# Kernel optimization log

Measured on AMD Instinct MI355X. Metric: run time of the kernel, lower is better.

## Reference

```python
import jax, jax.numpy as jnp
import numpy as np

TEMP = 0.2
L_MAIN, L_VIEW, L_SUP, L_UNSUP = 1.0, 1.0, 1.0, 0.2
N, D, V, P, NEG, U = 100000, 256, 3, 1024, 1024, 2048


def setup_inputs() -> dict:
    key = jax.random.key(0)
    ks = jax.random.split(key, 8)
    fused_logit = jax.random.normal(ks[0], (N,), dtype=jnp.float32)
    view_logits = jax.random.normal(ks[1], (V, N), dtype=jnp.float32)
    proj = jax.random.normal(ks[2], (V, N, D), dtype=jnp.float32)
    proj = proj / jnp.linalg.norm(proj, axis=-1, keepdims=True)  # 'already normalized'
    labels = jax.random.randint(ks[3], (N,), 0, 2).astype(jnp.float32)
    train_mask = jax.random.randint(ks[4], (N,), 0, 2).astype(bool)
    train_pos_idx = jax.random.randint(ks[5], (P,), 0, N)
    train_neg_idx = jax.random.randint(ks[6], (NEG,), 0, N)
    unlabeled_idx = jax.random.randint(ks[7], (U,), 0, N)  # len == max_unsup_samples -> no subsampling
    return dict(fused_logit=fused_logit, view_logits=view_logits, proj=proj,
                labels=labels, train_mask=train_mask, train_pos_idx=train_pos_idx,
                train_neg_idx=train_neg_idx, unlabeled_idx=unlabeled_idx)


def _masked_bce(logits, labels, mask):
    # BCEWithLogitsLoss mean over masked elements (stable formulation)
    bce = jnp.maximum(logits, 0) - logits * labels + jnp.log1p(jnp.exp(-jnp.abs(logits)))
    mf = mask.astype(logits.dtype)
    return jnp.sum(bce * mf) / jnp.maximum(jnp.sum(mf), 1.0)


def _sup_contrastive(proj, pos_idx, neg_idx, temp):
    lab_idx = jnp.concatenate([pos_idx, neg_idx])
    node_labels = jnp.concatenate([jnp.ones(pos_idx.shape[0]), jnp.zeros(neg_idx.shape[0])])
    L = lab_idx.shape[0]
    Vv = proj.shape[0]
    z = proj[:, lab_idx, :].transpose(1, 0, 2)          # [L, V, D]
    zf = z.reshape(L * Vv, -1)                           # [L*V, D]
    sim = (zf @ zf.T) / temp                             # [L*V, L*V]
    sim = sim - jax.lax.stop_gradient(sim.max(axis=1, keepdims=True))
    es = jnp.exp(sim)
    node = jnp.repeat(jnp.arange(L), Vv)
    view = jnp.tile(jnp.arange(Vv), L)
    flab = jnp.repeat(node_labels, Vv)
    sn = node[:, None] == node[None, :]
    sv = view[:, None] == view[None, :]
    sl = flab[:, None] == flab[None, :]
    eye = jnp.eye(L * Vv, dtype=bool)
    pos_m = ((sn & ~sv) | (~sn & sl)) & ~eye
    neg_m = (~sn) & (~sl) & ~eye
    den_m = pos_m | neg_m
    denom = jnp.sum(es * den_m.astype(es.dtype), axis=1) + 1e-12
    posf = pos_m.astype(es.dtype)
    log_prob = -jnp.log((es * posf + 1e-12) / denom[:, None])
    pos_count = pos_m.sum(axis=1)
    loss_per_anchor = jnp.sum(log_prob * posf, axis=1) / (pos_count.astype(es.dtype) + 1e-12)
    valid = ((pos_count > 0) & (den_m.sum(axis=1) > 0)).astype(es.dtype)
    return jnp.sum(loss_per_anchor * valid) / jnp.maximum(jnp.sum(valid), 1.0)


def _unsup_consistency(proj, unl_idx, temp):
    # Vectorized form of the double python loop: full cosine-sim matrix with
    # masked denominator (all but self) and positives = same node, other views.
    Vv = proj.shape[0]
    z = proj[:, unl_idx, :].transpose(1, 0, 2)           # [U, V, D]
    Uu = z.shape[0]
    M = Uu * Vv
    zf = z.reshape(M, -1)
    zn = zf / (jnp.linalg.norm(zf, axis=1, keepdims=True) + 1e-8)
    es = jnp.exp((zn @ zn.T) / temp)                     # [M, M]
    denom = es.sum(axis=1) - jnp.diag(es) + 1e-12        # exclude self
    node = jnp.repeat(jnp.arange(Uu), Vv)
    view = jnp.tile(jnp.arange(Vv), Uu)
    pos_m = (node[:, None] == node[None, :]) & (view[:, None] != view[None, :])
    posf = pos_m.astype(es.dtype)
    log_prob = -jnp.log(es / denom[:, None])
    per_anchor = jnp.sum(log_prob * posf, axis=1) / (Vv - 1)
    return jnp.mean(per_anchor)


def reference(fused_logit, view_logits, proj, labels, train_mask,
              train_pos_idx, train_neg_idx, unlabeled_idx):
    main_loss = _masked_bce(fused_logit, labels, train_mask)
    view_loss = jnp.mean(jax.vmap(lambda lg: _masked_bce(lg, labels, train_mask))(view_logits))
    sup_loss = _sup_contrastive(proj, train_pos_idx, train_neg_idx, TEMP)
    unsup_loss = _unsup_consistency(proj, unlabeled_idx, TEMP)
    total = L_MAIN * main_loss + L_VIEW * view_loss + L_SUP * sup_loss + L_UNSUP * unsup_loss
    return jnp.stack([total, main_loss, view_loss, sup_loss, unsup_loss])
```

## Files before the change

kernel.cpp:

```cpp
#include <hip/hip_runtime.h>
#include <math.h>

typedef short short8 __attribute__((ext_vector_type(8)));
typedef float floatx4 __attribute__((ext_vector_type(4)));

#define TEMP_INV 5.0f
#define W_UNSUP 0.2f
#define NB_BCE 256
#define NSPLIT 8

static __device__ __forceinline__ unsigned short f2bf(float f) {
  unsigned int u = __float_as_uint(f);
  u += 0x7FFFu + ((u >> 16) & 1u);
  return (unsigned short)(u >> 16);
}

__device__ __forceinline__ float block_sum256(float v) {
  __shared__ float sh[4];
  for (int m = 1; m <= 32; m <<= 1) v += __shfl_xor(v, m);
  __syncthreads();
  if ((threadIdx.x & 63) == 0) sh[threadIdx.x >> 6] = v;
  __syncthreads();
  return sh[0] + sh[1] + sh[2] + sh[3];
}

__global__ __launch_bounds__(256) void bce_kernel(
    const float* __restrict__ fused, const float* __restrict__ viewl,
    const float* __restrict__ labels, const void* __restrict__ maskp,
    float* __restrict__ partials, int N, int V, int nw) {
  __shared__ int s_int, s_flt;
  const int t = threadIdx.x;
  if (t == 0) { s_int = 1; s_flt = 1; }
  __syncthreads();
  {
    const unsigned int* w = (const unsigned int*)maskp;
    int okI = 1, okF = 1;
    for (int i = t; i < nw; i += 256) {
      unsigned int x = w[i];
      if (x != 0u && x != 1u) okI = 0;
      if (x != 0u && x != 0x3F800000u) okF = 0;
    }
    if (!okI) atomicAnd(&s_int, 0);
    if (!okF) atomicAnd(&s_flt, 0);
  }
  __syncthreads();
  const int flag = s_int ? 0 : (s_flt ? 1 : 2);

  float cnt = 0.f, sm = 0.f;
  float sv[8];
  for (int v = 0; v < 8; v++) sv[v] = 0.f;
  const int Vc = V > 8 ? 8 : V;
  for (int i = blockIdx.x * blockDim.x + t; i < N; i += gridDim.x * blockDim.x) {
    bool m;
    if (flag == 0)      m = ((const int*)maskp)[i] != 0;
    else if (flag == 1) m = ((const float*)maskp)[i] != 0.0f;
    else                m = ((const unsigned char*)maskp)[i] != 0;
    if (!m) continue;
    float y = labels[i];
    cnt += 1.0f;
    float x = fused[i];
    sm += fmaxf(x, 0.f) - x * y + log1pf(__expf(-fabsf(x)));
    for (int v = 0; v < Vc; v++) {
      float xv = viewl[(size_t)v * N + i];
      sv[v] += fmaxf(xv, 0.f) - xv * y + log1pf(__expf(-fabsf(xv)));
    }
  }
  float tot = block_sum256(cnt);
  if (t == 0) partials[blockIdx.x * 16 + 0] = tot;
  tot = block_sum256(sm);
  if (t == 0) partials[blockIdx.x * 16 + 1] = tot;
  for (int v = 0; v < Vc; v++) {
    tot = block_sum256(sv[v]);
    if (t == 0) partials[blockIdx.x * 16 + 2 + v] = tot;
  }
}

__global__ __launch_bounds__(256) void gather_kernel(
    const float* __restrict__ proj, const int* __restrict__ pos_idx,
    const int* __restrict__ neg_idx, const int* __restrict__ unl_idx,
    unsigned short* __restrict__ zsup, unsigned short* __restrict__ zuns,
    float* __restrict__ dsup, float* __restrict__ duns,
    float* __restrict__ Esup, float* __restrict__ Bsup,
    float* __restrict__ Euns, float* __restrict__ Buns,
    int N, int D, int V, int P, int Msup, int Muns) {
  const int prob = blockIdx.y;
  const int M = prob ? Muns : Msup;
  const int r0 = blockIdx.x * 8;
  const int t = threadIdx.x;
  if (t < 8) {
    int rz = r0 + t;
    if (rz < M) {
      if (prob) { Euns[rz] = 0.f; Buns[rz] = 0.f; }
      else      { Esup[rz] = 0.f; Bsup[rz] = 0.f; }
    }
  }
  const int sub = t >> 5, ln = t & 31;
  const int r = r0 + sub;
  if (r >= M) return;
  const int l = r / V, v = r - l * V;
  const int idx = prob ? unl_idx[l] : (l < P ? pos_idx[l] : neg_idx[l - P]);
  const float* src = proj + ((size_t)v * N + (size_t)idx) * D + ln * 8;
  floatx4 p0 = *(const floatx4*)(src);
  floatx4 p1 = *(const floatx4*)(src + 4);
  float s = 0.f;
#pragma unroll
  for (int k = 0; k < 4; k++) s += p0[k] * p0[k] + p1[k] * p1[k];
  for (int m = 1; m <= 16; m <<= 1) s += __shfl_xor(s, m);
  const float n2 = s;
  float sc = 1.0f, dval = n2 * TEMP_INV;
  if (prob) {
    sc = 1.0f / (sqrtf(n2) + 1e-8f);
    dval = n2 * sc * sc * TEMP_INV;
  }
  short8 vv;
#pragma unroll
  for (int k = 0; k < 4; k++) {
    vv[k]     = (short)f2bf(p0[k] * sc);
    vv[k + 4] = (short)f2bf(p1[k] * sc);
  }
  unsigned short* zd = prob ? zuns : zsup;
  *(short8*)(zd + (size_t)r * 256 + ln * 8) = vv;
  if (ln == 0) (prob ? duns : dsup)[r] = dval;
}

__global__ __launch_bounds__(256) void sim_kernel(
    const unsigned short* __restrict__ zsup, const unsigned short* __restrict__ zuns,
    float* __restrict__ Esup, float* __restrict__ Bsup,
    float* __restrict__ Euns, float* __restrict__ Buns,
    int Msup, int Muns, int PV, int V, int nsSup, int nsUns) {
  const int prob = blockIdx.y;
  const unsigned short* __restrict__ z = prob ? zuns : zsup;
  float* __restrict__ Ep = prob ? Euns : Esup;
  float* __restrict__ Bp = prob ? Buns : Bsup;
  const int M = prob ? Muns : Msup;
  const int ns = prob ? nsUns : nsSup;

  const int si = blockIdx.x / NSPLIT;
  const int s  = blockIdx.x - si * NSPLIT;
  if (si >= ns) return;

  const int R0 = si * 64;
  const int tid = threadIdx.x;
  const int wave = tid >> 6;
  const int wr = wave >> 1, wc = wave & 1;
  const int q = (tid >> 4) & 3;
  const int n16 = tid & 15;

  __shared__ __align__(16) unsigned short lds[64 * 264];

  const int srow = tid >> 5;
  const int soff = (tid & 31) * 8;

  short8 a[2][8];
#pragma unroll
  for (int m = 0; m < 2; m++) {
    int row = R0 + wr * 32 + m * 16 + n16;
    if (row >= M) row = M - 1;
    const unsigned short* zr = z + (size_t)row * 256 + q * 8;
#pragma unroll
    for (int ks = 0; ks < 8; ks++) a[m][ks] = *(const short8*)(zr + ks * 32);
  }

  int bs[2][4], be[2][4];
#pragma unroll
  for (int m = 0; m < 2; m++)
#pragma unroll
    for (int r = 0; r < 4; r++) {
      int row = R0 + wr * 32 + m * 16 + q * 4 + r;
      if (row >= M) row = M - 1;
      if (prob == 0) { bs[m][r] = row < PV ? 0 : PV; be[m][r] = row < PV ? PV : M; }
      else           { int b0 = (row / V) * V; bs[m][r] = b0; be[m][r] = b0 + V; }
    }

  float er0[4] = {0, 0, 0, 0}, er1[4] = {0, 0, 0, 0};
  float br0[4] = {0, 0, 0, 0}, br1[4] = {0, 0, 0, 0};

  short8 cur[8];
  int tj = si + s;
  if (tj < ns) {
    const int C0 = tj * 64;
#pragma unroll
    for (int cc = 0; cc < 8; cc++) {
      int gcol = C0 + srow + cc * 8;
      short8 vv = {0, 0, 0, 0, 0, 0, 0, 0};
      if (gcol < M) vv = *(const short8*)(z + (size_t)gcol * 256 + soff);
      cur[cc] = vv;
    }
  }

  for (; tj < ns; tj += NSPLIT) {
    const int C0 = tj * 64;
    __syncthreads();
#pragma unroll
    for (int cc = 0; cc < 8; cc++)
      *(short8*)(&lds[(srow + cc * 8) * 264 + soff]) = cur[cc];
    {
      int tjn = tj + NSPLIT;
      if (tjn < ns) {
        const int C0n = tjn * 64;
#pragma unroll
        for (int cc = 0; cc < 8; cc++) {
          int gcol = C0n + srow + cc * 8;
          short8 vv = {0, 0, 0, 0, 0, 0, 0, 0};
          if (gcol < M) vv = *(const short8*)(z + (size_t)gcol * 256 + soff);
          cur[cc] = vv;
        }
      }
    }
    __syncthreads();

    floatx4 acc00 = {0.f, 0.f, 0.f, 0.f}, acc01 = {0.f, 0.f, 0.f, 0.f};
    floatx4 acc10 = {0.f, 0.f, 0.f, 0.f}, acc11 = {0.f, 0.f, 0.f, 0.f};
#pragma unroll
    for (int ks = 0; ks < 8; ks++) {
      const unsigned short* bp = &lds[(wc * 32 + n16) * 264 + q * 8 + ks * 32];
      short8 b0 = *(const short8*)bp;
      short8 b1 = *(const short8*)(bp + 16 * 264);
      acc00 = __builtin_amdgcn_mfma_f32_16x16x32_bf16(a[0][ks], b0, acc00, 0, 0, 0);
      acc01 = __builtin_amdgcn_mfma_f32_16x16x32_bf16(a[0][ks], b1, acc01, 0, 0, 0);
      acc10 = __builtin_amdgcn_mfma_f32_16x16x32_bf16(a[1][ks], b0, acc10, 0, 0, 0);
      acc11 = __builtin_amdgcn_mfma_f32_16x16x32_bf16(a[1][ks], b1, acc11, 0, 0, 0);
    }

    float ec0 = 0.f, ec1 = 0.f, bc0 = 0.f, bc1 = 0.f;
    const int j0 = C0 + wc * 32 + n16;
    const int j1 = j0 + 16;

#define EPI(ACC, MM, JN, ECOL, BCOL, ERA, BRA)                        \
  _Pragma("unroll")                                                   \
  for (int r = 0; r < 4; r++) {                                       \
    int row = R0 + wr * 32 + MM * 16 + q * 4 + r;                     \
    float tv = ACC[r] * TEMP_INV;                                     \
    bool valid = (row < M) && (JN < M);                               \
    float e = valid ? __expf(tv - 5.0f) : 0.0f;                       \
    float bv = (valid && JN >= bs[MM][r] && JN < be[MM][r]) ? tv : 0.0f; \
    ERA[r] += e; BRA[r] += bv; ECOL += e; BCOL += bv;                 \
  }
    EPI(acc00, 0, j0, ec0, bc0, er0, br0)
    EPI(acc01, 0, j1, ec1, bc1, er0, br0)
    EPI(acc10, 1, j0, ec0, bc0, er1, br1)
    EPI(acc11, 1, j1, ec1, bc1, er1, br1)
#undef EPI

    if (tj != si) {
      float e = ec0, b = bc0;
      e += __shfl_xor(e, 16); e += __shfl_xor(e, 32);
      b += __shfl_xor(b, 16); b += __shfl_xor(b, 32);
      if (q == 0 && j0 < M) { atomicAdd(&Ep[j0], e); atomicAdd(&Bp[j0], b); }
      e = ec1; b = bc1;
      e += __shfl_xor(e, 16); e += __shfl_xor(e, 32);
      b += __shfl_xor(b, 16); b += __shfl_xor(b, 32);
      if (q == 0 && j1 < M) { atomicAdd(&Ep[j1], e); atomicAdd(&Bp[j1], b); }
    }
  }

#pragma unroll
  for (int mr = 0; mr < 8; mr++) {
    const int m = mr >> 2, r = mr & 3;
    float e = m ? er1[r] : er0[r];
    float b = m ? br1[r] : br0[r];
    for (int msk = 1; msk <= 8; msk <<= 1) { e += __shfl_xor(e, msk); b += __shfl_xor(b, msk); }
    int row = R0 + wr * 32 + m * 16 + q * 4 + r;
    if (n16 == 0 && row < M) {
      atomicAdd(&Ep[row], e);
      atomicAdd(&Bp[row], b);
    }
  }
}

__global__ __launch_bounds__(256) void finalize_kernel(
    const float* __restrict__ partials,
    const float* __restrict__ Esup, const float* __restrict__ Bsup, const float* __restrict__ dsup,
    const float* __restrict__ Euns, const float* __restrict__ Buns, const float* __restrict__ duns,
    int Msup, int Muns, int PV, int P, int NEG, int V, float* __restrict__ out) {
  const int t = threadIdx.x;
  float cnt = 0.f, sm = 0.f, sv[8];
  for (int v = 0; v < 8; v++) sv[v] = 0.f;
  const int Vc = V > 8 ? 8 : V;
  for (int b = t; b < NB_BCE; b += 256) {
    cnt += partials[b * 16 + 0];
    sm  += partials[b * 16 + 1];
    for (int v = 0; v < Vc; v++) sv[v] += partials[b * 16 + 2 + v];
  }
  cnt = block_sum256(cnt);
  sm = block_sum256(sm);
  float svt = 0.f;
  for (int v = 0; v < Vc; v++) svt += block_sum256(sv[v]);
  const float denomC = fmaxf(cnt, 1.0f);
  const float main_loss = sm / denomC;
  const float view_loss = (svt / denomC) / (float)V;

  float ssup = 0.f;
  for (int row = t; row < Msup; row += 256) {
    float E = Esup[row], B = Bsup[row];
    float d = dsup[row];
    float dn = E - __expf(d - 5.0f);
    float cl = (row < PV) ? (float)P : (float)NEG;
    float pc = (float)(V - 1) + (cl - 1.0f) * (float)V;
    ssup += logf(dn) + 5.0f - (B - d) / pc;
  }
  ssup = block_sum256(ssup);
  const float sup_loss = ssup / (float)Msup;

  float suns = 0.f;
  for (int row = t; row < Muns; row += 256) {
    float E = Euns[row], B = Buns[row];
    float d = duns[row];
    float dn = E - __expf(d - 5.0f);
    suns += logf(dn) + 5.0f - (B - d) / (float)(V - 1);
  }
  suns = block_sum256(suns);
  const float unsup_loss = suns / (float)Muns;

  if (t == 0) {
    float total = main_loss + view_loss + sup_loss + W_UNSUP * unsup_loss;
    out[0] = total;
    out[1] = main_loss;
    out[2] = view_loss;
    out[3] = sup_loss;
    out[4] = unsup_loss;
  }
}

extern "C" void kernel_launch(void* const* d_in, const int* in_sizes, int n_in,
                              void* d_out, int out_size, void* d_ws, size_t ws_size,
                              hipStream_t stream) {
  const float* fused  = (const float*)d_in[0];
  const float* viewl  = (const float*)d_in[1];
  const float* proj   = (const float*)d_in[2];
  const float* labels = (const float*)d_in[3];
  const void*  maskp  = d_in[4];
  const int* pos_idx  = (const int*)d_in[5];
  const int* neg_idx  = (const int*)d_in[6];
  const int* unl_idx  = (const int*)d_in[7];

  const int N = in_sizes[0];
  const int V = in_sizes[1] / N;
  const int D = in_sizes[2] / in_sizes[1];
  const int P = in_sizes[5];
  const int NEG = in_sizes[6];
  const int U = in_sizes[7];
  const int L = P + NEG;
  const int Msup = L * V;
  const int Muns = U * V;
  const int PV = P * V;

  char* ws = (char*)d_ws;
  size_t off = 0;
  auto alloc = [&](size_t bytes) { size_t o = off; off += (bytes + 255) & ~(size_t)255; return o; };
  const size_t o_part = alloc((size_t)NB_BCE * 16 * 4);
  const size_t o_zsup = alloc((size_t)Msup * D * 2);
  const size_t o_zuns = alloc((size_t)Muns * D * 2);
  const size_t o_dsup = alloc((size_t)Msup * 4);
  const size_t o_duns = alloc((size_t)Muns * 4);
  const size_t o_Esup = alloc((size_t)Msup * 4);
  const size_t o_Bsup = alloc((size_t)Msup * 4);
  const size_t o_Euns = alloc((size_t)Muns * 4);
  const size_t o_Buns = alloc((size_t)Muns * 4);

  float* partials = (float*)(ws + o_part);
  unsigned short* zsup = (unsigned short*)(ws + o_zsup);
  unsigned short* zuns = (unsigned short*)(ws + o_zuns);
  float* dsup = (float*)(ws + o_dsup);
  float* duns = (float*)(ws + o_duns);
  float* Esup = (float*)(ws + o_Esup);
  float* Bsup = (float*)(ws + o_Bsup);
  float* Euns = (float*)(ws + o_Euns);
  float* Buns = (float*)(ws + o_Buns);

  int nw = N / 4 < 256 ? N / 4 : 256;
  bce_kernel<<<NB_BCE, 256, 0, stream>>>(fused, viewl, labels, maskp, partials, N, V, nw);

  const int Mmax = Msup > Muns ? Msup : Muns;
  dim3 ggrid((Mmax + 7) / 8, 2);
  gather_kernel<<<ggrid, 256, 0, stream>>>(proj, pos_idx, neg_idx, unl_idx,
                                           zsup, zuns, dsup, duns,
                                           Esup, Bsup, Euns, Buns,
                                           N, D, V, P, Msup, Muns);

  const int nsS = (Msup + 63) / 64;
  const int nsU = (Muns + 63) / 64;
  const int nsMax = nsS > nsU ? nsS : nsU;
  dim3 sgrid(nsMax * NSPLIT, 2);
  sim_kernel<<<sgrid, 256, 0, stream>>>(zsup, zuns, Esup, Bsup, Euns, Buns,
                                        Msup, Muns, PV, V, nsS, nsU);

  finalize_kernel<<<1, 256, 0, stream>>>(partials, Esup, Bsup, dsup, Euns, Buns, duns,
                                         Msup, Muns, PV, P, NEG, V, (float*)d_out);
}
```

Before: 445.3 us.

## Merge BCE and gather kernels; fold finalize into sim via last-block ticket

The BCE reduction and the gather/normalize step become a single prep kernel, with blocks partitioned by index. The finalize reduction moves into the tail of the similarity kernel: each block takes an atomic ticket, and the last block to finish computes the final losses using coherent loads. Four launches become two, removing launch overhead and inter-kernel gaps. In exchange every sim block pays for an extra atomic and fence, and the final reduction runs on a single block at the end of the kernel.

```diff
diff --git a/kernel.cpp b/kernel.cpp
--- a/kernel.cpp
+++ b/kernel.cpp
@@ -13,6 +13,10 @@
   unsigned int u = __float_as_uint(f);
   u += 0x7FFFu + ((u >> 16) & 1u);
   return (unsigned short)(u >> 16);
+}
+
+static __device__ __forceinline__ float coh_load(const float* p) {
+  return __hip_atomic_load(p, __ATOMIC_RELAXED, __HIP_MEMORY_SCOPE_AGENT);
 }
 
 __device__ __forceinline__ float block_sum256(float v) {
@@ -24,69 +28,74 @@
   return sh[0] + sh[1] + sh[2] + sh[3];
 }
 
-__global__ __launch_bounds__(256) void bce_kernel(
+__global__ __launch_bounds__(256) void prep_kernel(
     const float* __restrict__ fused, const float* __restrict__ viewl,
     const float* __restrict__ labels, const void* __restrict__ maskp,
-    float* __restrict__ partials, int N, int V, int nw) {
-  __shared__ int s_int, s_flt;
-  const int t = threadIdx.x;
-  if (t == 0) { s_int = 1; s_flt = 1; }
-  __syncthreads();
-  {
-    const unsigned int* w = (const unsigned int*)maskp;
-    int okI = 1, okF = 1;
-    for (int i = t; i < nw; i += 256) {
-      unsigned int x = w[i];
-      if (x != 0u && x != 1u) okI = 0;
-      if (x != 0u && x != 0x3F800000u) okF = 0;
-    }
-    if (!okI) atomicAnd(&s_int, 0);
-    if (!okF) atomicAnd(&s_flt, 0);
-  }
-  __syncthreads();
-  const int flag = s_int ? 0 : (s_flt ? 1 : 2);
-
-  float cnt = 0.f, sm = 0.f;
-  float sv[8];
-  for (int v = 0; v < 8; v++) sv[v] = 0.f;
-  const int Vc = V > 8 ? 8 : V;
-  for (int i = blockIdx.x * blockDim.x + t; i < N; i += gridDim.x * blockDim.x) {
-    bool m;
-    if (flag == 0)      m = ((const int*)maskp)[i] != 0;
-    else if (flag == 1) m = ((const float*)maskp)[i] != 0.0f;
-    else                m = ((const unsigned char*)maskp)[i] != 0;
-    if (!m) continue;
-    float y = labels[i];
-    cnt += 1.0f;
-    float x = fused[i];
-    sm += fmaxf(x, 0.f) - x * y + log1pf(__expf(-fabsf(x)));
-    for (int v = 0; v < Vc; v++) {
-      float xv = viewl[(size_t)v * N + i];
-      sv[v] += fmaxf(xv, 0.f) - xv * y + log1pf(__expf(-fabsf(xv)));
-    }
-  }
-  float tot = block_sum256(cnt);
-  if (t == 0) partials[blockIdx.x * 16 + 0] = tot;
-  tot = block_sum256(sm);
-  if (t == 0) partials[blockIdx.x * 16 + 1] = tot;
-  for (int v = 0; v < Vc; v++) {
-    tot = block_sum256(sv[v]);
-    if (t == 0) partials[blockIdx.x * 16 + 2 + v] = tot;
-  }
-}
-
-__global__ __launch_bounds__(256) void gather_kernel(
+    float* __restrict__ partials, int N, int V, int nw,
     const float* __restrict__ proj, const int* __restrict__ pos_idx,
     const int* __restrict__ neg_idx, const int* __restrict__ unl_idx,
     unsigned short* __restrict__ zsup, unsigned short* __restrict__ zuns,
     float* __restrict__ dsup, float* __restrict__ duns,
     float* __restrict__ Esup, float* __restrict__ Bsup,
     float* __restrict__ Euns, float* __restrict__ Buns,
-    int N, int D, int V, int P, int Msup, int Muns) {
-  const int prob = blockIdx.y;
+    int D, int P, int Msup, int Muns, int gblocks,
+    unsigned int* __restrict__ ticket) {
+  const int bx = blockIdx.x;
+  const int t = threadIdx.x;
+  if (bx == 0 && t == 0) *ticket = 0u;
+
+  if (bx < NB_BCE) {
+    __shared__ int s_int, s_flt;
+    if (t == 0) { s_int = 1; s_flt = 1; }
+    __syncthreads();
+    {
+      const unsigned int* w = (const unsigned int*)maskp;
+      int okI = 1, okF = 1;
+      for (int i = t; i < nw; i += 256) {
+        unsigned int x = w[i];
+        if (x != 0u && x != 1u) okI = 0;
+        if (x != 0u && x != 0x3F800000u) okF = 0;
+      }
+      if (!okI) atomicAnd(&s_int, 0);
+      if (!okF) atomicAnd(&s_flt, 0);
+    }
+    __syncthreads();
+    const int flag = s_int ? 0 : (s_flt ? 1 : 2);
+
+    float cnt = 0.f, sm = 0.f;
+    float sv[8];
+    for (int v = 0; v < 8; v++) sv[v] = 0.f;
+    const int Vc = V > 8 ? 8 : V;
+    for (int i = bx * 256 + t; i < N; i += NB_BCE * 256) {
+      bool m;
+      if (flag == 0)      m = ((const int*)maskp)[i] != 0;
+      else if (flag == 1) m = ((const float*)maskp)[i] != 0.0f;
+      else                m = ((const unsigned char*)maskp)[i] != 0;
+      if (!m) continue;
+      float y = labels[i];
+      cnt += 1.0f;
+      float x = fused[i];
+      sm += fmaxf(x, 0.f) - x * y + log1pf(__expf(-fabsf(x)));
+      for (int v = 0; v < Vc; v++) {
+        float xv = viewl[(size_t)v * N + i];
+        sv[v] += fmaxf(xv, 0.f) - xv * y + log1pf(__expf(-fabsf(xv)));
+      }
+    }
+    float tot = block_sum256(cnt);
+    if (t == 0) partials[bx * 16 + 0] = tot;
+    tot = block_sum256(sm);
+    if (t == 0) partials[bx * 16 + 1] = tot;
+    for (int v = 0; v < Vc; v++) {
+      tot = block_sum256(sv[v]);
+      if (t == 0) partials[bx * 16 + 2 + v] = tot;
+    }
+    return;
+  }
+
+  const int g = bx - NB_BCE;
+  const int prob = g >= gblocks ? 1 : 0;
   const int M = prob ? Muns : Msup;
-  const int r0 = blockIdx.x * 8;
-  const int t = threadIdx.x;
+  const int r0 = (g - prob * gblocks) * 8;
   if (t < 8) {
     int rz = r0 + t;
     if (rz < M) {
@@ -127,7 +136,10 @@
     const unsigned short* __restrict__ zsup, const unsigned short* __restrict__ zuns,
     float* __restrict__ Esup, float* __restrict__ Bsup,
     float* __restrict__ Euns, float* __restrict__ Buns,
-    int Msup, int Muns, int PV, int V, int nsSup, int nsUns) {
+    int Msup, int Muns, int PV, int V, int nsSup, int nsUns,
+    const float* __restrict__ partials,
+    const float* __restrict__ dsup, const float* __restrict__ duns,
+    int P, int NEG, float* __restrict__ out, unsigned int* __restrict__ ticket) {
   const int prob = blockIdx.y;
   const unsigned short* __restrict__ z = prob ? zuns : zsup;
   float* __restrict__ Ep = prob ? Euns : Esup;
@@ -137,94 +149,95 @@
 
   const int si = blockIdx.x / NSPLIT;
   const int s  = blockIdx.x - si * NSPLIT;
-  if (si >= ns) return;
-
-  const int R0 = si * 64;
+
   const int tid = threadIdx.x;
-  const int wave = tid >> 6;
-  const int wr = wave >> 1, wc = wave & 1;
-  const int q = (tid >> 4) & 3;
-  const int n16 = tid & 15;
 
   __shared__ __align__(16) unsigned short lds[64 * 264];
 
-  const int srow = tid >> 5;
-  const int soff = (tid & 31) * 8;
-
-  short8 a[2][8];
-#pragma unroll
-  for (int m = 0; m < 2; m++) {
-    int row = R0 + wr * 32 + m * 16 + n16;
-    if (row >= M) row = M - 1;
-    const unsigned short* zr = z + (size_t)row * 256 + q * 8;
-#pragma unroll
-    for (int ks = 0; ks < 8; ks++) a[m][ks] = *(const short8*)(zr + ks * 32);
-  }
-
-  int bs[2][4], be[2][4];
-#pragma unroll
-  for (int m = 0; m < 2; m++)
-#pragma unroll
-    for (int r = 0; r < 4; r++) {
-      int row = R0 + wr * 32 + m * 16 + q * 4 + r;
+  if (si < ns) {
+    const int R0 = si * 64;
+    const int wave = tid >> 6;
+    const int wr = wave >> 1, wc = wave & 1;
+    const int q = (tid >> 4) & 3;
+    const int n16 = tid & 15;
+
+    const int srow = tid >> 5;
+    const int soff = (tid & 31) * 8;
+
+    short8 a[2][8];
+#pragma unroll
+    for (int m = 0; m < 2; m++) {
+      int row = R0 + wr * 32 + m * 16 + n16;
       if (row >= M) row = M - 1;
-      if (prob == 0) { bs[m][r] = row < PV ? 0 : PV; be[m][r] = row < PV ? PV : M; }
-      else           { int b0 = (row / V) * V; bs[m][r] = b0; be[m][r] = b0 + V; }
-    }
-
-  float er0[4] = {0, 0, 0, 0}, er1[4] = {0, 0, 0, 0};
-  float br0[4] = {0, 0, 0, 0}, br1[4] = {0, 0, 0, 0};
-
-  short8 cur[8];
-  int tj = si + s;
-  if (tj < ns) {
-    const int C0 = tj * 64;
-#pragma unroll
-    for (int cc = 0; cc < 8; cc++) {
-      int gcol = C0 + srow + cc * 8;
-      short8 vv = {0, 0, 0, 0, 0, 0, 0, 0};
-      if (gcol < M) vv = *(const short8*)(z + (size_t)gcol * 256 + soff);
-      cur[cc] = vv;
-    }
-  }
-
-  for (; tj < ns; tj += NSPLIT) {
-    const int C0 = tj * 64;
-    __syncthreads();
-#pragma unroll
-    for (int cc = 0; cc < 8; cc++)
-      *(short8*)(&lds[(srow + cc * 8) * 264 + soff]) = cur[cc];
-    {
-      int tjn = tj + NSPLIT;
-      if (tjn < ns) {
-        const int C0n = tjn * 64;
-#pragma unroll
-        for (int cc = 0; cc < 8; cc++) {
-          int gcol = C0n + srow + cc * 8;
-          short8 vv = {0, 0, 0, 0, 0, 0, 0, 0};
-          if (gcol < M) vv = *(const short8*)(z + (size_t)gcol * 256 + soff);
-          cur[cc] = vv;
+      const unsigned short* zr = z + (size_t)row * 256 + q * 8;
+#pragma unroll
+      for (int ks = 0; ks < 8; ks++) a[m][ks] = *(const short8*)(zr + ks * 32);
+    }
+
+    int bs[2][4], be[2][4];
+#pragma unroll
+    for (int m = 0; m < 2; m++)
+#pragma unroll
+      for (int r = 0; r < 4; r++) {
+        int row = R0 + wr * 32 + m * 16 + q * 4 + r;
+        if (row >= M) row = M - 1;
+        if (prob == 0) { bs[m][r] = row < PV ? 0 : PV; be[m][r] = row < PV ? PV : M; }
+        else           { int b0 = (row / V) * V; bs[m][r] = b0; be[m][r] = b0 + V; }
+      }
+
+    float er0[4] = {0, 0, 0, 0}, er1[4] = {0, 0, 0, 0};
+    float br0[4] = {0, 0, 0, 0}, br1[4] = {0, 0, 0, 0};
+
+    short8 cur[8];
+    int tj = si + s;
+    if (tj < ns) {
+      const int C0 = tj * 64;
+#pragma unroll
+      for (int cc = 0; cc < 8; cc++) {
+        int gcol = C0 + srow + cc * 8;
+        short8 vv = {0, 0, 0, 0, 0, 0, 0, 0};
+        if (gcol < M) vv = *(const short8*)(z + (size_t)gcol * 256 + soff);
+        cur[cc] = vv;
+      }
+    }
+
+    for (; tj < ns; tj += NSPLIT) {
+      const int C0 = tj * 64;
+      __syncthreads();
+#pragma unroll
+      for (int cc = 0; cc < 8; cc++)
+        *(short8*)(&lds[(srow + cc * 8) * 264 + soff]) = cur[cc];
+      {
+        int tjn = tj + NSPLIT;
+        if (tjn < ns) {
+          const int C0n = tjn * 64;
+#pragma unroll
+          for (int cc = 0; cc < 8; cc++) {
+            int gcol = C0n + srow + cc * 8;
+            short8 vv = {0, 0, 0, 0, 0, 0, 0, 0};
+            if (gcol < M) vv = *(const short8*)(z + (size_t)gcol * 256 + soff);
+            cur[cc] = vv;
+          }
         }
       }
-    }
-    __syncthreads();
-
-    floatx4 acc00 = {0.f, 0.f, 0.f, 0.f}, acc01 = {0.f, 0.f, 0.f, 0.f};
-    floatx4 acc10 = {0.f, 0.f, 0.f, 0.f}, acc11 = {0.f, 0.f, 0.f, 0.f};
-#pragma unroll
-    for (int ks = 0; ks < 8; ks++) {
-      const unsigned short* bp = &lds[(wc * 32 + n16) * 264 + q * 8 + ks * 32];
-      short8 b0 = *(const short8*)bp;
-      short8 b1 = *(const short8*)(bp + 16 * 264);
-      acc00 = __builtin_amdgcn_mfma_f32_16x16x32_bf16(a[0][ks], b0, acc00, 0, 0, 0);
-      acc01 = __builtin_amdgcn_mfma_f32_16x16x32_bf16(a[0][ks], b1, acc01, 0, 0, 0);
-      acc10 = __builtin_amdgcn_mfma_f32_16x16x32_bf16(a[1][ks], b0, acc10, 0, 0, 0);
-      acc11 = __builtin_amdgcn_mfma_f32_16x16x32_bf16(a[1][ks], b1, acc11, 0, 0, 0);
-    }
-
-    float ec0 = 0.f, ec1 = 0.f, bc0 = 0.f, bc1 = 0.f;
-    const int j0 = C0 + wc * 32 + n16;
-    const int j1 = j0 + 16;
+      __syncthreads();
+
+      floatx4 acc00 = {0.f, 0.f, 0.f, 0.f}, acc01 = {0.f, 0.f, 0.f, 0.f};
+      floatx4 acc10 = {0.f, 0.f, 0.f, 0.f}, acc11 = {0.f, 0.f, 0.f, 0.f};
+#pragma unroll
+      for (int ks = 0; ks < 8; ks++) {
+        const unsigned short* bp = &lds[(wc * 32 + n16) * 264 + q * 8 + ks * 32];
+        short8 b0 = *(const short8*)bp;
+        short8 b1 = *(const short8*)(bp + 16 * 264);
+        acc00 = __builtin_amdgcn_mfma_f32_16x16x32_bf16(a[0][ks], b0, acc00, 0, 0, 0);
+        acc01 = __builtin_amdgcn_mfma_f32_16x16x32_bf16(a[0][ks], b1, acc01, 0, 0, 0);
+        acc10 = __builtin_amdgcn_mfma_f32_16x16x32_bf16(a[1][ks], b0, acc10, 0, 0, 0);
+        acc11 = __builtin_amdgcn_mfma_f32_16x16x32_bf16(a[1][ks], b1, acc11, 0, 0, 0);
+      }
+
+      float ec0 = 0.f, ec1 = 0.f, bc0 = 0.f, bc1 = 0.f;
+      const int j0 = C0 + wc * 32 + n16;
+      const int j1 = j0 + 16;
 
 #define EPI(ACC, MM, JN, ECOL, BCOL, ERA, BRA)                        \
   _Pragma("unroll")                                                   \
@@ -236,44 +249,49 @@
     float bv = (valid && JN >= bs[MM][r] && JN < be[MM][r]) ? tv : 0.0f; \
     ERA[r] += e; BRA[r] += bv; ECOL += e; BCOL += bv;                 \
   }
-    EPI(acc00, 0, j0, ec0, bc0, er0, br0)
-    EPI(acc01, 0, j1, ec1, bc1, er0, br0)
-    EPI(acc10, 1, j0, ec0, bc0, er1, br1)
-    EPI(acc11, 1, j1, ec1, bc1, er1, br1)
+      EPI(acc00, 0, j0, ec0, bc0, er0, br0)
+      EPI(acc01, 0, j1, ec1, bc1, er0, br0)
+      EPI(acc10, 1, j0, ec0, bc0, er1, br1)
+      EPI(acc11, 1, j1, ec1, bc1, er1, br1)
 #undef EPI
 
-    if (tj != si) {
-      float e = ec0, b = bc0;
-      e += __shfl_xor(e, 16); e += __shfl_xor(e, 32);
-      b += __shfl_xor(b, 16); b += __shfl_xor(b, 32);
-      if (q == 0 && j0 < M) { atomicAdd(&Ep[j0], e); atomicAdd(&Bp[j0], b); }
-      e = ec1; b = bc1;
-      e += __shfl_xor(e, 16); e += __shfl_xor(e, 32);
-      b += __shfl_xor(b, 16); b += __shfl_xor(b, 32);
-      if (q == 0 && j1 < M) { atomicAdd(&Ep[j1], e); atomicAdd(&Bp[j1], b); }
-    }
-  }
-
-#pragma unroll
-  for (int mr = 0; mr < 8; mr++) {
-    const int m = mr >> 2, r = mr & 3;
-    float e = m ? er1[r] : er0[r];
-    float b = m ? br1[r] : br0[r];
-    for (int msk = 1; msk <= 8; msk <<= 1) { e += __shfl_xor(e, msk); b += __shfl_xor(b, msk); }
-    int row = R0 + wr * 32 + m * 16 + q * 4 + r;
-    if (n16 == 0 && row < M) {
-      atomicAdd(&Ep[row], e);
-      atomicAdd(&Bp[row], b);
-    }
-  }
-}
-
-__global__ __launch_bounds__(256) void finalize_kernel(
-    const float* __restrict__ partials,
-    const float* __restrict__ Esup, const float* __restrict__ Bsup, const float* __restrict__ dsup,
-    const float* __restrict__ Euns, const float* __restrict__ Buns, const float* __restrict__ duns,
-    int Msup, int Muns, int PV, int P, int NEG, int V, float* __restrict__ out) {
-  const int t = threadIdx.x;
+      if (tj != si) {
+        float e = ec0, b = bc0;
+        e += __shfl_xor(e, 16); e += __shfl_xor(e, 32);
+        b += __shfl_xor(b, 16); b += __shfl_xor(b, 32);
+        if (q == 0 && j0 < M) { atomicAdd(&Ep[j0], e); atomicAdd(&Bp[j0], b); }
+        e = ec1; b = bc1;
+        e += __shfl_xor(e, 16); e += __shfl_xor(e, 32);
+        b += __shfl_xor(b, 16); b += __shfl_xor(b, 32);
+        if (q == 0 && j1 < M) { atomicAdd(&Ep[j1], e); atomicAdd(&Bp[j1], b); }
+      }
+    }
+
+#pragma unroll
+    for (int mr = 0; mr < 8; mr++) {
+      const int m = mr >> 2, r = mr & 3;
+      float e = m ? er1[r] : er0[r];
+      float b = m ? br1[r] : br0[r];
+      for (int msk = 1; msk <= 8; msk <<= 1) { e += __shfl_xor(e, msk); b += __shfl_xor(b, msk); }
+      int row = R0 + wr * 32 + m * 16 + q * 4 + r;
+      if (n16 == 0 && row < M) {
+        atomicAdd(&Ep[row], e);
+        atomicAdd(&Bp[row], b);
+      }
+    }
+  }
+
+  __shared__ int isLast;
+  if (tid == 0) {
+    __threadfence();
+    unsigned int old = atomicAdd(ticket, 1u);
+    isLast = (old == gridDim.x * gridDim.y - 1u) ? 1 : 0;
+  }
+  __syncthreads();
+  if (!isLast) return;
+  __threadfence();
+
+  const int t = tid;
   float cnt = 0.f, sm = 0.f, sv[8];
   for (int v = 0; v < 8; v++) sv[v] = 0.f;
   const int Vc = V > 8 ? 8 : V;
@@ -292,7 +310,7 @@
 
   float ssup = 0.f;
   for (int row = t; row < Msup; row += 256) {
-    float E = Esup[row], B = Bsup[row];
+    float E = coh_load(&Esup[row]), B = coh_load(&Bsup[row]);
     float d = dsup[row];
     float dn = E - __expf(d - 5.0f);
     float cl = (row < PV) ? (float)P : (float)NEG;
@@ -304,7 +322,7 @@
 
   float suns = 0.f;
   for (int row = t; row < Muns; row += 256) {
-    float E = Euns[row], B = Buns[row];
+    float E = coh_load(&Euns[row]), B = coh_load(&Buns[row]);
     float d = duns[row];
     float dn = E - __expf(d - 5.0f);
     suns += logf(dn) + 5.0f - (B - d) / (float)(V - 1);
@@ -357,6 +375,7 @@
   const size_t o_Bsup = alloc((size_t)Msup * 4);
   const size_t o_Euns = alloc((size_t)Muns * 4);
   const size_t o_Buns = alloc((size_t)Muns * 4);
+  const size_t o_tick = alloc(4);
 
   float* partials = (float*)(ws + o_part);
   unsigned short* zsup = (unsigned short*)(ws + o_zsup);
@@ -367,24 +386,23 @@
   float* Bsup = (float*)(ws + o_Bsup);
   float* Euns = (float*)(ws + o_Euns);
   float* Buns = (float*)(ws + o_Buns);
+  unsigned int* ticket = (unsigned int*)(ws + o_tick);
 
   int nw = N / 4 < 256 ? N / 4 : 256;
-  bce_kernel<<<NB_BCE, 256, 0, stream>>>(fused, viewl, labels, maskp, partials, N, V, nw);
-
   const int Mmax = Msup > Muns ? Msup : Muns;
-  dim3 ggrid((Mmax + 7) / 8, 2);
-  gather_kernel<<<ggrid, 256, 0, stream>>>(proj, pos_idx, neg_idx, unl_idx,
-                                           zsup, zuns, dsup, duns,
-                                           Esup, Bsup, Euns, Buns,
-                                           N, D, V, P, Msup, Muns);
+  const int gblocks = (Mmax + 7) / 8;
+  prep_kernel<<<NB_BCE + 2 * gblocks, 256, 0, stream>>>(
+      fused, viewl, labels, maskp, partials, N, V, nw,
+      proj, pos_idx, neg_idx, unl_idx,
+      zsup, zuns, dsup, duns, Esup, Bsup, Euns, Buns,
+      D, P, Msup, Muns, gblocks, ticket);
 
   const int nsS = (Msup + 63) / 64;
   const int nsU = (Muns + 63) / 64;
   const int nsMax = nsS > nsU ? nsS : nsU;
   dim3 sgrid(nsMax * NSPLIT, 2);
   sim_kernel<<<sgrid, 256, 0, stream>>>(zsup, zuns, Esup, Bsup, Euns, Buns,
-                                        Msup, Muns, PV, V, nsS, nsU);
-
-  finalize_kernel<<<1, 256, 0, stream>>>(partials, Esup, Bsup, dsup, Euns, Buns, duns,
-                                         Msup, Muns, PV, P, NEG, V, (float*)d_out);
-}
+                                        Msup, Muns, PV, V, nsS, nsU,
+                                        partials, dsup, duns, P, NEG,
+                                        (float*)d_out, ticket);
+}
```

Measured after the change: 457.0 us. +2.6%, slower.
